# Kernel optimization log

Measured on AMD Instinct MI355X. Metric: run time of the kernel, lower is better.

Reference implementation:

```python
import jax, jax.numpy as jnp
import numpy as np

N = 20000        # atoms in batch
E = 640000       # edges (avg degree 32)
NG = 1000        # molecules (graphs)
H = 128          # hidden_channels = num_filters
G = 50           # num_gaussians
L = 6            # num_interactions
CUTOFF = 10.0
LOG2 = float(np.log(2.0))


def ssp(x):
    # ShiftedSoftplus: softplus(x) - log(2)
    return jax.nn.softplus(x) - jnp.asarray(LOG2, x.dtype)


def setup_inputs() -> dict:
    key = jax.random.key(0)
    ks = jax.random.split(key, 16)
    pos = jax.random.normal(ks[0], (N, 3), dtype=jnp.float32) * 3.0
    z = jax.random.randint(ks[1], (N,), 1, 100)  # avoid padding_idx 0
    batch = jnp.sort(jax.random.randint(ks[2], (N,), 0, NG))
    edge_index = jax.random.randint(ks[3], (2, E), 0, N)
    # avoid self-loops (zero distance -> nan grad of norm)
    row, col = edge_index[0], edge_index[1]
    col = jnp.where(col == row, (col + 1) % N, col)
    edge_index = jnp.stack([row, col])

    def lin(k, fi, fo, stacked=False):
        shape = (L, fi, fo) if stacked else (fi, fo)
        return (jax.random.normal(k, shape, dtype=jnp.float32) / np.sqrt(fi)).astype(jnp.float32)

    emb = jax.random.normal(ks[4], (100, H), dtype=jnp.float32)
    emb = emb.at[0].set(0.0)  # padding_idx=0
    inp = {
        "pos": pos, "z": z, "batch": batch, "edge_index": edge_index,
        "emb": emb,
        "mlp_w1": lin(ks[5], G, H, True), "mlp_b1": jnp.zeros((L, H), jnp.float32),
        "mlp_w2": lin(ks[6], H, H, True), "mlp_b2": jnp.zeros((L, H), jnp.float32),
        "aw_w": lin(ks[7], H, H, True), "aw_b": jnp.zeros((L, H), jnp.float32),
        "out_w1": lin(ks[8], H, H, True), "out_b1": jnp.zeros((L, H), jnp.float32),
        "out_w2": lin(ks[9], H, H, True), "out_b2": jnp.zeros((L, H), jnp.float32),
        "head_w1": lin(ks[10], H, H // 2), "head_b1": jnp.zeros((H // 2,), jnp.float32),
        "head_w2": lin(ks[11], H // 2, 1), "head_b2": jnp.zeros((1,), jnp.float32),
    }
    return inp


def reference(pos, z, batch, edge_index, emb,
              mlp_w1, mlp_b1, mlp_w2, mlp_b2,
              aw_w, aw_b, out_w1, out_b1, out_w2, out_b2,
              head_w1, head_b1, head_w2, head_b2):
    row, col = edge_index[0], edge_index[1]
    # edge distances
    diff = pos[row] - pos[col]                       # [E,3]
    d = jnp.sqrt(jnp.sum(diff * diff, axis=-1))      # [E]
    # Gaussian smearing
    offset = jnp.linspace(0.0, CUTOFF, G)
    coeff = -0.5 / (offset[1] - offset[0]) ** 2
    ea = jnp.exp(coeff * (d[:, None] - offset[None, :]) ** 2)  # [E,G]
    # cosine cutoff
    C = 0.5 * (jnp.cos(d * jnp.pi / CUTOFF) + 1.0)             # [E]

    h = emb[z]                                                 # [N,H]
    for l in range(L):
        hw = h @ aw_w[l] + aw_b[l]                             # atom-wise linear
        W = ssp(ssp(ea @ mlp_w1[l] + mlp_b1[l]) @ mlp_w2[l] + mlp_b2[l]) * C[:, None]  # [E,H]
        msg = hw[row] * W                                      # gather + filter
        conv = jax.ops.segment_sum(msg, col, num_segments=N)   # scatter-add to targets
        upd = ssp(conv @ out_w1[l] + out_b1[l]) @ out_w2[l] + out_b2[l]
        h = h + upd                                            # residual
    y = ssp(h @ head_w1 + head_b1) @ head_w2 + head_b2         # [N,1]
    return jax.ops.segment_sum(y, batch, num_segments=NG)      # [NG,1]
```

## Files before the change

### kernel.cpp

```cpp
#include <hip/hip_runtime.h>
#include <math.h>

#define HID 128
#define NG_GAUSS 50
#define TBL_P 4096
#define TBL_DMAX 12.8f
#define TBL_DT (TBL_DMAX / (float)TBL_P)
#define TBL_INV_DT ((float)TBL_P / TBL_DMAX)
#define PI_F 3.14159265358979323846f
#define NB 16
#define BSH 11

typedef short bf16x8 __attribute__((ext_vector_type(8)));
typedef float f32x4 __attribute__((ext_vector_type(4)));

__device__ __forceinline__ float ssp_f(float x) {
  float e = __expf(-fabsf(x));
  return fmaxf(x, 0.f) + __logf(1.f + e) - 0.69314718055994530942f;
}
__device__ __forceinline__ unsigned short f2bf(float x) {
  unsigned u = __float_as_uint(x);
  unsigned r = (u + 0x7FFFu + ((u >> 16) & 1u)) >> 16;
  return (unsigned short)r;
}
__device__ __forceinline__ float bf2f_s(unsigned short v) {
  return __uint_as_float((unsigned)v << 16);
}

__global__ __launch_bounds__(256) void k_edge_pre(
    const float* __restrict__ pos, const int* __restrict__ ei,
    int E, int* __restrict__ epack, int* __restrict__ deg)
{
  int e = blockIdx.x * 256 + threadIdx.x;
  if (e >= E) return;
  int r = ei[e];
  int c = ei[E + e];
  float dx = pos[3*r+0] - pos[3*c+0];
  float dy = pos[3*r+1] - pos[3*c+1];
  float dz = pos[3*r+2] - pos[3*c+2];
  float d = sqrtf(dx*dx + dy*dy + dz*dz);
  int i0 = (int)(d * TBL_INV_DT + 0.5f);
  if (i0 >= TBL_P) { epack[e] = -1; return; }
  epack[e] = (r << 13) | i0;
  atomicAdd(&deg[c * NB + (r >> BSH)], 1);
}

__global__ __launch_bounds__(1024) void k_scan1(
    const int* __restrict__ deg, int* __restrict__ ptr,
    int* __restrict__ bsum, int M)
{
  __shared__ int wsum[16];
  int base = blockIdx.x * 2048;
  int t = threadIdx.x;
  int i0 = base + 2 * t;
  int v0 = (i0 < M) ? deg[i0] : 0;
  int v1 = (i0 + 1 < M) ? deg[i0 + 1] : 0;
  int s = v0 + v1;
  int lane = t & 63, w = t >> 6;
  int ps = s;
  for (int o = 1; o < 64; o <<= 1) { int x = __shfl_up(ps, o); if (lane >= o) ps += x; }
  if (lane == 63) wsum[w] = ps;
  __syncthreads();
  if (w == 0 && lane < 16) {
    int v = wsum[lane];
    int pv = v;
    for (int o = 1; o < 16; o <<= 1) { int x = __shfl_up(pv, o); if (lane >= o) pv += x; }
    wsum[lane] = pv - v;
  }
  __syncthreads();
  int ex = wsum[w] + ps - s;
  if (i0 < M) ptr[i0] = ex;
  if (i0 + 1 < M) ptr[i0 + 1] = ex + v0;
  if (t == 1023) bsum[blockIdx.x] = ex + s;
}

__global__ __launch_bounds__(1024) void k_scan2(int* __restrict__ bsum, int G)
{
  __shared__ int wsum[16];
  int t = threadIdx.x;
  int s = (t < G) ? bsum[t] : 0;
  int lane = t & 63, w = t >> 6;
  int ps = s;
  for (int o = 1; o < 64; o <<= 1) { int x = __shfl_up(ps, o); if (lane >= o) ps += x; }
  if (lane == 63) wsum[w] = ps;
  __syncthreads();
  if (w == 0 && lane < 16) {
    int v = wsum[lane];
    int pv = v;
    for (int o = 1; o < 16; o <<= 1) { int x = __shfl_up(pv, o); if (lane >= o) pv += x; }
    wsum[lane] = pv - v;
  }
  __syncthreads();
  int ex = wsum[w] + ps - s;
  if (t < G) bsum[t] = ex;
  if (t == G - 1) bsum[G] = ex + s;
}

__global__ __launch_bounds__(1024) void k_scan3(
    int* __restrict__ ptr, int* __restrict__ cursor,
    const int* __restrict__ bsum, int M, int G)
{
  int base = blockIdx.x * 2048;
  int t = threadIdx.x;
  int add = bsum[blockIdx.x];
  int i0 = base + 2 * t;
  if (i0 < M) { int v = ptr[i0] + add; ptr[i0] = v; cursor[i0] = v; }
  if (i0 + 1 < M) { int v = ptr[i0 + 1] + add; ptr[i0 + 1] = v; cursor[i0 + 1] = v; }
  if (blockIdx.x == 0 && t == 0) ptr[M] = bsum[G];
}

__global__ __launch_bounds__(256) void k_csr_scatter(
    const int* __restrict__ col, const int* __restrict__ epack,
    int* __restrict__ cursor, int* __restrict__ csr, int E)
{
  int e = blockIdx.x * 256 + threadIdx.x;
  if (e >= E) return;
  int p = epack[e];
  if (p < 0) return;
  int c = col[e];
  int idx = c * NB + ((p >> 13) >> BSH);
  int slot = atomicAdd(&cursor[idx], 1);
  csr[slot] = p;
}

__global__ __launch_bounds__(256) void k_wprep(
    const float* __restrict__ aw_w, const float* __restrict__ out_w1,
    const float* __restrict__ out_w2, const float* __restrict__ mlp_w2,
    const float* __restrict__ mlp_w1, const float* __restrict__ head_w1,
    unsigned short* __restrict__ awt, unsigned short* __restrict__ o1t,
    unsigned short* __restrict__ o2t, unsigned short* __restrict__ m2t,
    unsigned short* __restrict__ m1t, unsigned short* __restrict__ hwt)
{
  __shared__ float Wl[64][132];
  int l = blockIdx.x, t = blockIdx.y;
  int k0 = blockIdx.z * 64;
  const float* src; unsigned short* dst; int K; int NCOL = 128;
  switch (t) {
    case 0:  src = aw_w;   dst = awt; K = 128; break;
    case 1:  src = out_w1; dst = o1t; K = 128; break;
    case 2:  src = out_w2; dst = o2t; K = 128; break;
    case 3:  src = mlp_w2; dst = m2t; K = 128; break;
    case 4:  src = mlp_w1; dst = m1t; K = NG_GAUSS; break;
    default:
      if (l) return;
      src = head_w1; dst = hwt; K = 128; NCOL = 64; break;
  }
  src += (long)l * K * NCOL;
  dst += (long)l * 128 * 128;
  const int tid = threadIdx.x;
  for (int idx = tid; idx < 64 * 128; idx += 256) {
    int kk = idx >> 7, n = idx & 127;
    int k = k0 + kk;
    Wl[kk][n] = (k < K && n < NCOL) ? src[(long)k * NCOL + n] : 0.f;
  }
  __syncthreads();
  for (int idx = tid; idx < 128 * 8; idx += 256) {
    int n = idx >> 3, pl = idx & 7;
    int p = (k0 >> 3) + pl;
    int q = p ^ (n & 7);
    int kk = (q << 3) - k0;
    ushort4 lo = make_ushort4(f2bf(Wl[kk+0][n]), f2bf(Wl[kk+1][n]),
                              f2bf(Wl[kk+2][n]), f2bf(Wl[kk+3][n]));
    ushort4 hi = make_ushort4(f2bf(Wl[kk+4][n]), f2bf(Wl[kk+5][n]),
                              f2bf(Wl[kk+6][n]), f2bf(Wl[kk+7][n]));
    *(ushort4*)(dst + ((long)n << 7) + (p << 3)) = lo;
    *(ushort4*)(dst + ((long)n << 7) + (p << 3) + 4) = hi;
  }
}

__global__ void k_ea_build(unsigned short* __restrict__ EA)
{
  int p = blockIdx.x;
  int g = threadIdx.x;
  float v = 0.f;
  if (g < NG_GAUSS) {
    float step = 10.0f / 49.0f;
    float off = g * step;
    float coeff = -0.5f / (step * step);
    float t = p * TBL_DT - off;
    v = __expf(coeff * t * t);
  }
  EA[p * 128 + g] = f2bf(v);
}

__global__ void k_emb2bf(const float* __restrict__ emb,
                         unsigned short* __restrict__ embb, int NE)
{
  int idx = blockIdx.x * 256 + threadIdx.x;
  if (idx >= NE * 16) return;
  const float* er = emb + (long)idx * 8;
  float4 lo = *(const float4*)er;
  float4 hi = *(const float4*)(er + 4);
  alignas(16) unsigned short u[8];
  u[0]=f2bf(lo.x); u[1]=f2bf(lo.y); u[2]=f2bf(lo.z); u[3]=f2bf(lo.w);
  u[4]=f2bf(hi.x); u[5]=f2bf(hi.y); u[6]=f2bf(hi.z); u[7]=f2bf(hi.w);
  *(int4*)(embb + (long)idx * 8) = *(int4*)u;
}

__global__ __launch_bounds__(256) void k_h_init(
    const unsigned short* __restrict__ embb,
    const unsigned short* __restrict__ embw,
    const int* __restrict__ z,
    unsigned short* __restrict__ h, unsigned short* __restrict__ hw, int N)
{
  int idx = blockIdx.x * 256 + threadIdx.x;
  if (idx >= N * 16) return;
  int n = idx >> 4, c = idx & 15;
  long src = (long)z[n] * 128 + (c << 3);
  long dst = (long)n * 128 + (c << 3);
  *(int4*)(h + dst) = *(const int4*)(embb + src);
  *(int4*)(hw + dst) = *(const int4*)(embw + src);
}

__global__ __launch_bounds__(256) void k_fused(
    const unsigned short* __restrict__ X, long xstr,
    const unsigned short* __restrict__ Wa, long wastr,
    const float* __restrict__ ba, long bastr,
    const unsigned short* __restrict__ Wb, long wbstr,
    const float* __restrict__ bb, long bbstr,
    unsigned short* __restrict__ R,
    int r_write,
    void* __restrict__ out1, long o1str, int o1_bf16, int actB, int mulC,
    float dscale,
    const unsigned short* __restrict__ Wc, const float* __restrict__ bc,
    unsigned short* __restrict__ out2,
    const float* __restrict__ hw2, const float* __restrict__ hb2,
    const int* __restrict__ batchp, float* __restrict__ outp,
    int M)
{
  __shared__ unsigned short Xs[32][128];
  __shared__ unsigned short Wbuf[128][128];

  const int l = blockIdx.y;
  const int m0 = blockIdx.x * 32;
  const int tid = threadIdx.x;
  const unsigned short* Xb = X + (long)l * xstr;

  for (int idx = tid; idx < 512; idx += 256) {
    int r = idx >> 4, c = idx & 15;
    int m = m0 + r;
    int4 v = make_int4(0, 0, 0, 0);
    if (m < M) v = *(const int4*)(Xb + (long)m * 128 + c * 8);
    *(int4*)&Xs[r][(c ^ (r & 7)) << 3] = v;
  }
  {
    const unsigned short* W0 = Wa ? (Wa + (long)l * wastr) : (Wb + (long)l * wbstr);
    const int4* s = (const int4*)W0;
    int4* d = (int4*)Wbuf;
    for (int i = tid; i < 2048; i += 256) d[i] = s[i];
  }
  __syncthreads();

  const int wv = tid >> 6, lane = tid & 63;
  const int wr = wv >> 1, wc = wv & 1;
  const int lr = lane & 15, lk = lane >> 4;
  const int arow = (wr << 4) | lr;

  f32x4 acc[4];
  auto zacc = [&]() {
#pragma unroll
    for (int i = 0; i < 4; ++i)
#pragma unroll
      for (int j = 0; j < 4; ++j) acc[i][j] = 0.f;
  };
  auto gemm = [&]() {
#pragma unroll
    for (int kc = 0; kc < 4; ++kc) {
      int q = (kc << 2) | lk;
      bf16x8 a = *(const bf16x8*)&Xs[arow][(q ^ (arow & 7)) << 3];
#pragma unroll
      for (int nt = 0; nt < 4; ++nt) {
        int n = (wc << 6) | (nt << 4) | lr;
        bf16x8 b = *(const bf16x8*)(&Wbuf[0][0] + n * 128 + ((q ^ (n & 7)) << 3));
        acc[nt] = __builtin_amdgcn_mfma_f32_16x16x32_bf16(a, b, acc[nt], 0, 0, 0);
      }
    }
  };

  if (Wa) {
    const float* bab = ba + (long)l * bastr;
    zacc();
    gemm();
    __syncthreads();
#pragma unroll
    for (int nt = 0; nt < 4; ++nt) {
      int col = (wc << 6) | (nt << 4) | lr;
      float bv = bab[col];
#pragma unroll
      for (int r2 = 0; r2 < 4; ++r2) {
        int row = (wr << 4) | (lk << 2) | r2;
        float v2 = ssp_f(acc[nt][r2] + bv);
        int cch = col >> 3;
        Xs[row][((cch ^ (row & 7)) << 3) | (col & 7)] = f2bf(v2);
      }
    }
    {
      const int4* s = (const int4*)(Wb + (long)l * wbstr);
      int4* d = (int4*)Wbuf;
      for (int i = tid; i < 2048; i += 256) d[i] = s[i];
    }
    __syncthreads();
  }

  const float* bbb = bb + (long)l * bbstr;
  zacc();
  gemm();
  __syncthreads();

#pragma unroll
  for (int nt = 0; nt < 4; ++nt) {
    int col = (wc << 6) | (nt << 4) | lr;
    float bv = bbb[col];
#pragma unroll
    for (int r2 = 0; r2 < 4; ++r2) {
      int row = (wr << 4) | (lk << 2) | r2;
      int m = m0 + row;
      float v2 = acc[nt][r2] + bv;
      if (actB) v2 = ssp_f(v2);
      if (R && m < M) {
        v2 += bf2f_s(R[(long)m * 128 + col]);
        if (r_write) R[(long)m * 128 + col] = f2bf(v2);
      }
      if (mulC) {
        float d = (float)m * dscale;
        v2 *= 0.5f * (__cosf(d * (PI_F / 10.0f)) + 1.0f);
      }
      if (m < M && out1) {
        if (o1_bf16)
          ((unsigned short*)out1)[(long)l * o1str + (long)m * 128 + col] = f2bf(v2);
        else
          ((float*)out1)[(long)l * o1str + (long)m * 128 + col] = v2;
      }
      if (Wc) {
        int cch = col >> 3;
        Xs[row][((cch ^ (row & 7)) << 3) | (col & 7)] = f2bf(v2);
      }
    }
  }

  if (Wc) {
    {
      const int4* s = (const int4*)Wc;
      int4* d = (int4*)Wbuf;
      for (int i = tid; i < 2048; i += 256) d[i] = s[i];
    }
    __syncthreads();
    zacc();
    gemm();
    if (hw2) {
      if (wc == 0) {
        float b1v[4], w2v[4];
#pragma unroll
        for (int nt = 0; nt < 4; ++nt) {
          int col = (nt << 4) | lr;
          b1v[nt] = bc[col];
          w2v[nt] = hw2[col];
        }
        float bias2 = hb2[0];
#pragma unroll
        for (int r2 = 0; r2 < 4; ++r2) {
          float sv = 0.f;
#pragma unroll
          for (int nt = 0; nt < 4; ++nt)
            sv += ssp_f(acc[nt][r2] + b1v[nt]) * w2v[nt];
          sv += __shfl_xor(sv, 1);
          sv += __shfl_xor(sv, 2);
          sv += __shfl_xor(sv, 4);
          sv += __shfl_xor(sv, 8);
          if (lr == 0) {
            int m = m0 + (wr << 4) + (lk << 2) + r2;
            if (m < M) atomicAdd(&outp[batchp[m]], sv + bias2);
          }
        }
      }
    } else {
#pragma unroll
      for (int nt = 0; nt < 4; ++nt) {
        int col = (wc << 6) | (nt << 4) | lr;
        float bv = bc[col];
#pragma unroll
        for (int r2 = 0; r2 < 4; ++r2) {
          int row = (wr << 4) | (lk << 2) | r2;
          int m = m0 + row;
          if (m < M)
            out2[(long)m * 128 + col] = f2bf(acc[nt][r2] + bv);
        }
      }
    }
  }
}

__global__ __launch_bounds__(256) void k_conv(
    const int* __restrict__ csr, const int* __restrict__ ptr,
    const unsigned short* __restrict__ T, const unsigned short* __restrict__ hw,
    unsigned short* __restrict__ convb, int N)
{
  int wid = __builtin_amdgcn_readfirstlane((blockIdx.x * 256 + threadIdx.x) >> 6);
  int lane = threadIdx.x & 63;
  if (wid >= N) return;
  int s = __builtin_amdgcn_readfirstlane(ptr[wid * NB]);
  int e = __builtin_amdgcn_readfirstlane(ptr[wid * NB + NB]);
  const int la = lane << 1;
  float ax[8], ay[8];
#pragma unroll
  for (int i = 0; i < 8; ++i) { ax[i] = 0.f; ay[i] = 0.f; }
  int j = s;
  if (j + 8 <= e) {
    int cc[8];
#pragma unroll
    for (int i = 0; i < 8; ++i) cc[i] = __builtin_amdgcn_readfirstlane(csr[j + i]);
    for (; j + 16 <= e; j += 8) {
      unsigned tv[8], hv[8];
#pragma unroll
      for (int i = 0; i < 8; ++i) {
        unsigned pr = (unsigned)cc[i];
        tv[i] = *(const unsigned*)(T + ((size_t)(pr & 4095u) << 7) + la);
        hv[i] = *(const unsigned*)(hw + ((size_t)(pr >> 13) << 7) + la);
      }
#pragma unroll
      for (int i = 0; i < 8; ++i) cc[i] = __builtin_amdgcn_readfirstlane(csr[j + 8 + i]);
#pragma unroll
      for (int i = 0; i < 8; ++i) {
        float w0 = __uint_as_float(tv[i] << 16), w1 = __uint_as_float(tv[i] & 0xffff0000u);
        float h0 = __uint_as_float(hv[i] << 16), h1 = __uint_as_float(hv[i] & 0xffff0000u);
        ax[i] = fmaf(w0, h0, ax[i]); ay[i] = fmaf(w1, h1, ay[i]);
      }
    }
    {
      unsigned tv[8], hv[8];
#pragma unroll
      for (int i = 0; i < 8; ++i) {
        unsigned pr = (unsigned)cc[i];
        tv[i] = *(const unsigned*)(T + ((size_t)(pr & 4095u) << 7) + la);
        hv[i] = *(const unsigned*)(hw + ((size_t)(pr >> 13) << 7) + la);
      }
#pragma unroll
      for (int i = 0; i < 8; ++i) {
        float w0 = __uint_as_float(tv[i] << 16), w1 = __uint_as_float(tv[i] & 0xffff0000u);
        float h0 = __uint_as_float(hv[i] << 16), h1 = __uint_as_float(hv[i] & 0xffff0000u);
        ax[i] = fmaf(w0, h0, ax[i]); ay[i] = fmaf(w1, h1, ay[i]);
      }
    }
    j += 8;
  }
  for (; j < e; ++j) {
    unsigned pr = (unsigned)__builtin_amdgcn_readfirstlane(csr[j]);
    unsigned tv = *(const unsigned*)(T + ((size_t)(pr & 4095u) << 7) + la);
    unsigned hv = *(const unsigned*)(hw + ((size_t)(pr >> 13) << 7) + la);
    float w0 = __uint_as_float(tv << 16), w1 = __uint_as_float(tv & 0xffff0000u);
    float h0 = __uint_as_float(hv << 16), h1 = __uint_as_float(hv & 0xffff0000u);
    ax[0] = fmaf(w0, h0, ax[0]); ay[0] = fmaf(w1, h1, ay[0]);
  }
  float axs = ((ax[0] + ax[1]) + (ax[2] + ax[3])) + ((ax[4] + ax[5]) + (ax[6] + ax[7]));
  float ays = ((ay[0] + ay[1]) + (ay[2] + ay[3])) + ((ay[4] + ay[5]) + (ay[6] + ay[7]));
  unsigned outw = (unsigned)f2bf(axs) | ((unsigned)f2bf(ays) << 16);
  *(unsigned*)(convb + ((size_t)wid << 7) + la) = outw;
}

extern "C" void kernel_launch(void* const* d_in, const int* in_sizes, int n_in,
                              void* d_out, int out_size, void* d_ws, size_t ws_size,
                              hipStream_t stream) {
  (void)n_in; (void)ws_size;
  const float* pos     = (const float*)d_in[0];
  const int*   z       = (const int*)d_in[1];
  const int*   batch   = (const int*)d_in[2];
  const int*   ei      = (const int*)d_in[3];
  const float* emb     = (const float*)d_in[4];
  const float* mlp_w1  = (const float*)d_in[5];
  const float* mlp_b1  = (const float*)d_in[6];
  const float* mlp_w2  = (const float*)d_in[7];
  const float* mlp_b2  = (const float*)d_in[8];
  const float* aw_w    = (const float*)d_in[9];
  const float* aw_b    = (const float*)d_in[10];
  const float* out_w1  = (const float*)d_in[11];
  const float* out_b1  = (const float*)d_in[12];
  const float* out_w2  = (const float*)d_in[13];
  const float* out_b2  = (const float*)d_in[14];
  const float* head_w1 = (const float*)d_in[15];
  const float* head_b1 = (const float*)d_in[16];
  const float* head_w2 = (const float*)d_in[17];
  const float* head_b2 = (const float*)d_in[18];

  const int N  = in_sizes[0] / 3;
  const int E  = in_sizes[3] / 2;
  const int NG = out_size;
  const int L  = in_sizes[5] / (NG_GAUSS * HID);
  const int NE = in_sizes[4] / HID;

  char* ws = (char*)d_ws;
  size_t off = 0;
  auto alloc = [&](size_t bytes) -> void* {
    off = (off + 255) & ~(size_t)255;
    void* p = ws + off;
    off += bytes;
    return p;
  };

  const size_t nh2 = (size_t)N * HID * 2;
  unsigned short* h = (unsigned short*)alloc(nh2 > (size_t)E * 4 ? nh2 : (size_t)E * 4);
  int* epack = (int*)h;
  unsigned short* hw    = (unsigned short*)alloc(nh2);
  unsigned short* convb = (unsigned short*)alloc(
      nh2 > (size_t)TBL_P * 128 * 2 ? nh2 : (size_t)TBL_P * 128 * 2);
  unsigned short* EA    = convb;
  int* csr = (int*)alloc((size_t)E * 4);
  unsigned short* T   = (unsigned short*)alloc((size_t)L * TBL_P * 128 * 2);
  unsigned short* awt = (unsigned short*)alloc((size_t)L * 16384 * 2);
  unsigned short* o1t = (unsigned short*)alloc((size_t)L * 16384 * 2);
  unsigned short* o2t = (unsigned short*)alloc((size_t)L * 16384 * 2);
  unsigned short* m2t = (unsigned short*)alloc((size_t)L * 16384 * 2);
  unsigned short* m1t = (unsigned short*)alloc((size_t)L * 16384 * 2);
  unsigned short* hwt = (unsigned short*)alloc((size_t)16384 * 2);
  unsigned short* embb = (unsigned short*)alloc((size_t)NE * 128 * 2);
  unsigned short* embw = (unsigned short*)alloc((size_t)NE * 128 * 2);
  int* deg    = (int*)alloc((size_t)N * NB * 4);
  int* ptr    = (int*)alloc(((size_t)N * NB + 1) * 4);
  int* cursor = (int*)alloc((size_t)N * NB * 4);
  int* bsum   = (int*)alloc((size_t)4096 * 4);

  const int M = N * NB;
  const int G = (M + 2047) / 2048;

  hipMemsetAsync(deg, 0, (size_t)M * 4, stream);
  hipMemsetAsync(d_out, 0, (size_t)NG * 4, stream);

  int egrid = (E + 255) / 256;
  k_edge_pre<<<egrid, 256, 0, stream>>>(pos, ei, E, epack, deg);
  k_scan1<<<G, 1024, 0, stream>>>(deg, ptr, bsum, M);
  k_scan2<<<1, 1024, 0, stream>>>(bsum, G);
  k_scan3<<<G, 1024, 0, stream>>>(ptr, cursor, bsum, M, G);
  k_csr_scatter<<<egrid, 256, 0, stream>>>(ei + E, epack, cursor, csr, E);

  k_wprep<<<dim3(L, 6, 2), 256, 0, stream>>>(aw_w, out_w1, out_w2, mlp_w2,
                                             mlp_w1, head_w1,
                                             awt, o1t, o2t, m2t, m1t, hwt);
  k_ea_build<<<TBL_P, 128, 0, stream>>>(EA);
  k_emb2bf<<<(NE * 16 + 255) / 256, 256, 0, stream>>>(emb, embb, NE);

  k_fused<<<dim3(TBL_P / 32, L), 256, 0, stream>>>(
      EA, 0L,
      m1t, 16384L, mlp_b1, 128L,
      m2t, 16384L, mlp_b2, 128L,
      (unsigned short*)0, 0,
      T, (long)TBL_P * 128, 1 , 1 , 1 , TBL_DT,
      (const unsigned short*)0, (const float*)0, (unsigned short*)0,
      (const float*)0, (const float*)0, (const int*)0, (float*)0,
      TBL_P);

  k_fused<<<dim3((NE + 31) / 32, 1), 256, 0, stream>>>(
      embb, 0L,
      (const unsigned short*)0, 0L, (const float*)0, 0L,
      awt, 0L, aw_b, 0L,
      (unsigned short*)0, 0,
      embw, 0L, 1 , 0, 0, 0.f,
      (const unsigned short*)0, (const float*)0, (unsigned short*)0,
      (const float*)0, (const float*)0, (const int*)0, (float*)0,
      NE);

  k_h_init<<<(N * 16 + 255) / 256, 256, 0, stream>>>(embb, embw, z, h, hw, N);

  const int ngrid = (N + 31) / 32;
  const int wgrid = (N * 64 + 255) / 256;

  for (int l = 0; l < L; ++l) {
    k_conv<<<wgrid, 256, 0, stream>>>(
        csr, ptr, T + (size_t)l * TBL_P * 128, hw, convb, N);
    const int last = (l + 1 == L);
    const unsigned short* Wc = last ? hwt : (awt + (size_t)(l + 1) * 16384);
    const float* bc = last ? head_b1 : (aw_b + (size_t)(l + 1) * 128);
    k_fused<<<dim3(ngrid, 1), 256, 0, stream>>>(
        convb, 0L,
        o1t + (size_t)l * 16384, 0L, out_b1 + (size_t)l * 128, 0L,
        o2t + (size_t)l * 16384, 0L, out_b2 + (size_t)l * 128, 0L,
        h, last ? 0 : 1 ,
        (void*)0, 0L, 0, 0 , 0, 0.f,
        Wc, bc, last ? (unsigned short*)0 : hw,
        last ? head_w2 : (const float*)0, last ? head_b2 : (const float*)0,
        last ? batch : (const int*)0, last ? (float*)d_out : (float*)0,
        N);
  }
}
```

Baseline: 362.5 us.

## Split each node's edge gather across two wavefronts with LDS reduction

The conv kernel now gives each destination node two wavefronts, each handling half of its edge list, and combines the partial sums through shared memory before writing the bf16 result. This doubles the number of waves in flight to hide gather latency on the table and hidden-state loads. In exchange it replaces the software-prefetched csr loop and scalar tail with a simpler masked 8-wide loop, which wastes loads on padded lanes and adds a block-wide barrier.

```diff
diff --git a/kernel.cpp b/kernel.cpp
--- a/kernel.cpp
+++ b/kernel.cpp
@@ -395,21 +395,30 @@
     const unsigned short* __restrict__ T, const unsigned short* __restrict__ hw,
     unsigned short* __restrict__ convb, int N)
 {
-  int wid = __builtin_amdgcn_readfirstlane((blockIdx.x * 256 + threadIdx.x) >> 6);
-  int lane = threadIdx.x & 63;
-  if (wid >= N) return;
-  int s = __builtin_amdgcn_readfirstlane(ptr[wid * NB]);
-  int e = __builtin_amdgcn_readfirstlane(ptr[wid * NB + NB]);
+  __shared__ float red[2][128];
+  const int lw = threadIdx.x >> 6;
+  const int gw = blockIdx.x * 4 + lw;
+  const int node = gw >> 1;
+  const int half = gw & 1;
+  const int lane = threadIdx.x & 63;
   const int la = lane << 1;
+
   float ax[8], ay[8];
 #pragma unroll
   for (int i = 0; i < 8; ++i) { ax[i] = 0.f; ay[i] = 0.f; }
-  int j = s;
-  if (j + 8 <= e) {
-    int cc[8];
-#pragma unroll
-    for (int i = 0; i < 8; ++i) cc[i] = __builtin_amdgcn_readfirstlane(csr[j + i]);
-    for (; j + 16 <= e; j += 8) {
+
+  if (node < N) {
+    int s = __builtin_amdgcn_readfirstlane(ptr[node * NB]);
+    int e = __builtin_amdgcn_readfirstlane(ptr[node * NB + NB]);
+    int hc = (e - s + 1) >> 1;
+    int js = s + half * hc;
+    int je = half ? e : (s + hc);
+    int emax = e - 1;
+    for (int j = js; j < je; j += 8) {
+      int cc[8];
+#pragma unroll
+      for (int i = 0; i < 8; ++i)
+        cc[i] = __builtin_amdgcn_readfirstlane(csr[min(j + i, emax)]);
       unsigned tv[8], hv[8];
 #pragma unroll
       for (int i = 0; i < 8; ++i) {
@@ -418,43 +427,28 @@
         hv[i] = *(const unsigned*)(hw + ((size_t)(pr >> 13) << 7) + la);
       }
 #pragma unroll
-      for (int i = 0; i < 8; ++i) cc[i] = __builtin_amdgcn_readfirstlane(csr[j + 8 + i]);
-#pragma unroll
       for (int i = 0; i < 8; ++i) {
-        float w0 = __uint_as_float(tv[i] << 16), w1 = __uint_as_float(tv[i] & 0xffff0000u);
-        float h0 = __uint_as_float(hv[i] << 16), h1 = __uint_as_float(hv[i] & 0xffff0000u);
-        ax[i] = fmaf(w0, h0, ax[i]); ay[i] = fmaf(w1, h1, ay[i]);
-      }
-    }
-    {
-      unsigned tv[8], hv[8];
-#pragma unroll
-      for (int i = 0; i < 8; ++i) {
-        unsigned pr = (unsigned)cc[i];
-        tv[i] = *(const unsigned*)(T + ((size_t)(pr & 4095u) << 7) + la);
-        hv[i] = *(const unsigned*)(hw + ((size_t)(pr >> 13) << 7) + la);
-      }
-#pragma unroll
-      for (int i = 0; i < 8; ++i) {
-        float w0 = __uint_as_float(tv[i] << 16), w1 = __uint_as_float(tv[i] & 0xffff0000u);
-        float h0 = __uint_as_float(hv[i] << 16), h1 = __uint_as_float(hv[i] & 0xffff0000u);
-        ax[i] = fmaf(w0, h0, ax[i]); ay[i] = fmaf(w1, h1, ay[i]);
-      }
-    }
-    j += 8;
-  }
-  for (; j < e; ++j) {
-    unsigned pr = (unsigned)__builtin_amdgcn_readfirstlane(csr[j]);
-    unsigned tv = *(const unsigned*)(T + ((size_t)(pr & 4095u) << 7) + la);
-    unsigned hv = *(const unsigned*)(hw + ((size_t)(pr >> 13) << 7) + la);
-    float w0 = __uint_as_float(tv << 16), w1 = __uint_as_float(tv & 0xffff0000u);
-    float h0 = __uint_as_float(hv << 16), h1 = __uint_as_float(hv & 0xffff0000u);
-    ax[0] = fmaf(w0, h0, ax[0]); ay[0] = fmaf(w1, h1, ay[0]);
+        bool ok = (j + i) < je;
+        float w0 = ok ? __uint_as_float(tv[i] << 16) : 0.f;
+        float w1 = ok ? __uint_as_float(tv[i] & 0xffff0000u) : 0.f;
+        float h0 = __uint_as_float(hv[i] << 16);
+        float h1 = __uint_as_float(hv[i] & 0xffff0000u);
+        ax[i] = fmaf(w0, h0, ax[i]);
+        ay[i] = fmaf(w1, h1, ay[i]);
+      }
+    }
   }
   float axs = ((ax[0] + ax[1]) + (ax[2] + ax[3])) + ((ax[4] + ax[5]) + (ax[6] + ax[7]));
   float ays = ((ay[0] + ay[1]) + (ay[2] + ay[3])) + ((ay[4] + ay[5]) + (ay[6] + ay[7]));
-  unsigned outw = (unsigned)f2bf(axs) | ((unsigned)f2bf(ays) << 16);
-  *(unsigned*)(convb + ((size_t)wid << 7) + la) = outw;
+
+  if (half == 1) { red[lw >> 1][la] = axs; red[lw >> 1][la + 1] = ays; }
+  __syncthreads();
+  if (half == 0 && node < N) {
+    axs += red[lw >> 1][la];
+    ays += red[lw >> 1][la + 1];
+    unsigned outw = (unsigned)f2bf(axs) | ((unsigned)f2bf(ays) << 16);
+    *(unsigned*)(convb + ((size_t)node << 7) + la) = outw;
+  }
 }
 
 extern "C" void kernel_launch(void* const* d_in, const int* in_sizes, int n_in,
@@ -560,10 +554,10 @@
   k_h_init<<<(N * 16 + 255) / 256, 256, 0, stream>>>(embb, embw, z, h, hw, N);
 
   const int ngrid = (N + 31) / 32;
-  const int wgrid = (N * 64 + 255) / 256;
+  const int cgrid = (2 * N + 3) / 4;
 
   for (int l = 0; l < L; ++l) {
-    k_conv<<<wgrid, 256, 0, stream>>>(
+    k_conv<<<cgrid, 256, 0, stream>>>(
         csr, ptr, T + (size_t)l * TBL_P * 128, hw, convb, N);
     const int last = (l + 1 == L);
     const unsigned short* Wc = last ? hwt : (awt + (size_t)(l + 1) * 16384);
```

Measured after the change: 409.7 us. 1.13x slower.
